# Performance work log

Measured on AMD Instinct MI355X. Metric: run time of the kernel, lower is better.

Reference implementation:

```python
import jax, jax.numpy as jnp
import numpy as np

ATTN_K = 64
H = 256  # seq_hidden_size


def setup_inputs() -> dict:
    key = jax.random.key(0)
    ks = jax.random.split(key, 10)
    N, Q = 1000000, 256
    return {
        "question": jax.random.normal(ks[0], (Q,), jnp.float32),
        "score": jax.random.uniform(ks[1], (), jnp.float32),
        "questions": jax.random.normal(ks[2], (N, Q), jnp.float32),
        "hs": jax.random.normal(ks[3], (N, H), jnp.float32),
        "W_score": jax.random.normal(ks[4], (1, Q + H), jnp.float32) * 0.05,
        "b_score": jax.random.normal(ks[5], (1,), jnp.float32) * 0.05,
        "W_ih": jax.random.normal(ks[6], (3 * H, 2 * Q), jnp.float32) * 0.05,
        "W_hh": jax.random.normal(ks[7], (3 * H, H), jnp.float32) * 0.05,
        "b_ih": jax.random.normal(ks[8], (3 * H,), jnp.float32) * 0.05,
        "b_hh": jax.random.normal(ks[9], (3 * H,), jnp.float32) * 0.05,
    }


def reference(question, score, questions, hs, W_score, b_score, W_ih, W_hh, b_ih, b_hh):
    # Attention over history: dot-product scores, top-k, softmax-weighted sum.
    alpha = questions @ question                      # [N]
    vals, idx = jax.lax.top_k(alpha, ATTN_K)          # [k], [k]
    w = jax.nn.softmax(vals)                          # softmax over the k selected scores
    attn_h = w @ hs[idx]                              # [H] weighted gather-sum

    # Score head on [question ; attn_h]
    pred_v = jnp.concatenate([question, attn_h])      # [Q+H]
    pred = W_score @ pred_v + b_score                 # [1]

    # GRU input: question gated by correctness of score
    right = (score >= 0.5).astype(question.dtype)
    x = jnp.concatenate([question * right, question * (1.0 - right)])  # [2Q]

    # Single GRU step (PyTorch gate ordering: r, z, n)
    h = hs[-1]                                        # [H]
    gx = W_ih @ x + b_ih                              # [3H]
    gh = W_hh @ h + b_hh                              # [3H]
    xr, xz, xn = gx[:H], gx[H:2 * H], gx[2 * H:]
    hr, hz, hn = gh[:H], gh[H:2 * H], gh[2 * H:]
    r = jax.nn.sigmoid(xr + hr)
    z = jax.nn.sigmoid(xz + hz)
    n = jnp.tanh(xn + r * hn)
    h_new = (1.0 - z) * n + z * h                     # [H]
    return pred, h_new
```

## Files before the change

### kernel.cpp

```cpp
#include <hip/hip_runtime.h>
#include <math.h>

#define Q 256
#define H 256
#define ATTN_K 64
#define CAP 4096
#define HBINS 4096

__device__ __forceinline__ unsigned f2k(float f) {
    unsigned u = __float_as_uint(f);
    return u ^ ((u & 0x80000000u) ? 0xFFFFFFFFu : 0x80000000u);
}

__global__ void k_setup(const float* __restrict__ question, const float* __restrict__ score,
                        const float* __restrict__ hs, const float* __restrict__ W_ih,
                        const float* __restrict__ W_hh, const float* __restrict__ b_ih,
                        const float* __restrict__ b_hh, float* __restrict__ gx,
                        float* __restrict__ gh, unsigned* __restrict__ hist,
                        unsigned* __restrict__ state, int N) {
    const int t = threadIdx.x;
    if (blockIdx.x < 16) hist[blockIdx.x * 256 + t] = 0u;
    if (blockIdx.x == 255 && t < 16) state[t] = 0u;

    const int o = blockIdx.x * 4 + (t >> 6);
    if (o >= 3 * H) return;
    const int lane = t & 63;
    const int off = (score[0] >= 0.5f) ? 0 : Q;
    const float4 q = *reinterpret_cast<const float4*>(question + lane * 4);
    const float4 h = *reinterpret_cast<const float4*>(hs + (size_t)(N - 1) * H + lane * 4);
    const float4 wx = *reinterpret_cast<const float4*>(W_ih + (size_t)o * (2 * Q) + off + lane * 4);
    const float4 wh = *reinterpret_cast<const float4*>(W_hh + (size_t)o * H + lane * 4);
    float px = wx.x * q.x + wx.y * q.y + wx.z * q.z + wx.w * q.w;
    float ph = wh.x * h.x + wh.y * h.y + wh.z * h.z + wh.w * h.w;
#pragma unroll
    for (int d = 32; d > 0; d >>= 1) {
        px += __shfl_xor(px, d, 64);
        ph += __shfl_xor(ph, d, 64);
    }
    if (lane == 0) {
        gx[o] = px + b_ih[o];
        gh[o] = ph + b_hh[o];
    }
}

__global__ __launch_bounds__(256) void k_alpha(const float* __restrict__ questions,
                                               const float* __restrict__ question,
                                               float* __restrict__ alpha, int N) {
    const int lane = threadIdx.x & 63;
    const int sub  = lane & 15;
    const int rg   = lane >> 4;
    const int wid  = (blockIdx.x * blockDim.x + threadIdx.x) >> 6;
    const int nw   = (gridDim.x * blockDim.x) >> 6;

    float4 q[4];
#pragma unroll
    for (int j = 0; j < 4; ++j)
        q[j] = *reinterpret_cast<const float4*>(question + j * 64 + sub * 4);

    for (int g = wid; g * 8 < N; g += nw) {
        const int rA = g * 8 + rg;
        const int rB = rA + 4;
        float pA = 0.f, pB = 0.f;
        if (rA < N) {
            const float* rowA = questions + (size_t)rA * Q + sub * 4;
#pragma unroll
            for (int j = 0; j < 4; ++j) {
                float4 x = *reinterpret_cast<const float4*>(rowA + j * 64);
                pA = fmaf(x.x, q[j].x, fmaf(x.y, q[j].y, fmaf(x.z, q[j].z, fmaf(x.w, q[j].w, pA))));
            }
        }
        if (rB < N) {
            const float* rowB = questions + (size_t)rB * Q + sub * 4;
#pragma unroll
            for (int j = 0; j < 4; ++j) {
                float4 x = *reinterpret_cast<const float4*>(rowB + j * 64);
                pB = fmaf(x.x, q[j].x, fmaf(x.y, q[j].y, fmaf(x.z, q[j].z, fmaf(x.w, q[j].w, pB))));
            }
        }
#pragma unroll
        for (int d = 1; d < 16; d <<= 1) {
            pA += __shfl_xor(pA, d, 64);
            pB += __shfl_xor(pB, d, 64);
        }
        if (sub == 0) {
            if (rA < N) alpha[rA] = pA;
            if (rB < N) alpha[rB] = pB;
        }
    }
}

__global__ __launch_bounds__(1024) void k_hist(const float* __restrict__ alpha,
                                               unsigned* __restrict__ hist, int N) {
    __shared__ unsigned hb[HBINS];
    const int t = threadIdx.x;
#pragma unroll
    for (int j = 0; j < HBINS / 1024; ++j) hb[t + j * 1024] = 0u;
    __syncthreads();

    const int n4 = N >> 2;
    const int stride = gridDim.x * blockDim.x;
    const float4* a4 = reinterpret_cast<const float4*>(alpha);
    for (int i = blockIdx.x * blockDim.x + t; i < n4; i += stride) {
        float4 a = a4[i];
        float v[4] = {a.x, a.y, a.z, a.w};
#pragma unroll
        for (int j = 0; j < 4; ++j) {
            int rel = (int)(f2k(v[j]) >> 19) - 4096;
            if (rel >= 0) atomicAdd(&hb[rel], 1u);
        }
    }
    if (blockIdx.x == 0 && t < (N & 3)) {
        float v = alpha[(n4 << 2) + t];
        int rel = (int)(f2k(v) >> 19) - 4096;
        if (rel >= 0) atomicAdd(&hb[rel], 1u);
    }
    __syncthreads();
#pragma unroll
    for (int j = 0; j < HBINS / 1024; ++j) {
        unsigned v = hb[t + j * 1024];
        if (v) atomicAdd(&hist[t + j * 1024], v);
    }
}

__global__ __launch_bounds__(1024) void k_scan(const unsigned* __restrict__ hist,
                                               unsigned* __restrict__ state) {
    __shared__ unsigned part[1024];
    __shared__ unsigned cum[1024];
    __shared__ int s_sh;
    const int t = threadIdx.x;

    {
        const int hi = 4095 - 4 * t;
        part[t] = hist[hi] + hist[hi - 1] + hist[hi - 2] + hist[hi - 3];
    }
    __syncthreads();
    cum[t] = part[t];
    __syncthreads();
    for (int d = 1; d < 1024; d <<= 1) {
        unsigned add = (t >= d) ? cum[t - d] : 0u;
        __syncthreads();
        if (t >= d) cum[t] += add;
        __syncthreads();
    }
    if (t == 0) s_sh = 1023;
    __syncthreads();
    if (cum[t] >= (unsigned)ATTN_K && (t == 0 || cum[t - 1] < (unsigned)ATTN_K)) s_sh = t;
    __syncthreads();
    if (t == 0) {
        const int s = s_sh;
        unsigned acc = (s > 0) ? cum[s - 1] : 0u;
        const int hi = 4095 - 4 * s;
        int tb = hi - 3;
        for (int b = hi; b >= hi - 3; --b) {
            acc += hist[b];
            if (acc >= (unsigned)ATTN_K) { tb = b; break; }
        }
        state[0] = (unsigned)(tb + 4096);
    }
}

__global__ void k_collect(const float* __restrict__ alpha, const unsigned* __restrict__ state,
                          float* __restrict__ cval, int* __restrict__ cidx,
                          unsigned* __restrict__ count, int N) {
    const int tau = (int)state[0];
    const int stride = gridDim.x * blockDim.x;
    const int n4 = N >> 2;
    const float4* a4 = reinterpret_cast<const float4*>(alpha);
    for (int i = blockIdx.x * blockDim.x + threadIdx.x; i < n4; i += stride) {
        float4 a = a4[i];
        float v[4] = {a.x, a.y, a.z, a.w};
#pragma unroll
        for (int j = 0; j < 4; ++j) {
            if ((int)(f2k(v[j]) >> 19) >= tau) {
                unsigned p = atomicAdd(count, 1u);
                if (p < CAP) { cval[p] = v[j]; cidx[p] = i * 4 + j; }
            }
        }
    }
    if (blockIdx.x == 0 && threadIdx.x < (N & 3)) {
        const int idx = (n4 << 2) + threadIdx.x;
        float v = alpha[idx];
        if ((int)(f2k(v) >> 19) >= tau) {
            unsigned p = atomicAdd(count, 1u);
            if (p < CAP) { cval[p] = v; cidx[p] = idx; }
        }
    }
}

__global__ void k_head(const float* __restrict__ question, const float* __restrict__ hs,
                       const float* __restrict__ W_score, const float* __restrict__ b_score,
                       const unsigned* __restrict__ state, const float* __restrict__ cval,
                       const int* __restrict__ cidx, const float* __restrict__ gx,
                       const float* __restrict__ gh, float* __restrict__ out, int N) {
    __shared__ float lv[CAP];
    __shared__ int li[CAP];
    __shared__ float sw[ATTN_K];
    __shared__ int si[ATTN_K];
    __shared__ float red[256];
    const int t = threadIdx.x;
    const int C = min((int)state[1], CAP);

    for (int i = t; i < C; i += 256) { lv[i] = cval[i]; li[i] = cidx[i]; }
    __syncthreads();

    if (t < 64) {
        for (int k = 0; k < ATTN_K; ++k) {
            float bv = -INFINITY;
            int bi = 0x7fffffff;
            int bp = -1;
            for (int i = t; i < C; i += 64) {
                float v = lv[i];
                int id = li[i];
                if (v > bv || (v == bv && id < bi)) { bv = v; bi = id; bp = i; }
            }
#pragma unroll
            for (int d = 32; d > 0; d >>= 1) {
                float ov = __shfl_xor(bv, d, 64);
                int oi = __shfl_xor(bi, d, 64);
                int op = __shfl_xor(bp, d, 64);
                if (ov > bv || (ov == bv && oi < bi)) { bv = ov; bi = oi; bp = op; }
            }
            if (t == 0) {
                sw[k] = bv;
                si[k] = (bi == 0x7fffffff) ? 0 : bi;
                if (bp >= 0) lv[bp] = -INFINITY;
            }
        }
        float m = sw[0];
        float e = expf(sw[t] - m);
        float ssum = e;
#pragma unroll
        for (int d = 32; d > 0; d >>= 1) ssum += __shfl_xor(ssum, d, 64);
        sw[t] = e / ssum;
    }
    __syncthreads();

    float aj = 0.f;
    for (int k = 0; k < ATTN_K; ++k) {
        aj = fmaf(sw[k], hs[(size_t)si[k] * H + t], aj);
    }

    red[t] = W_score[t] * question[t] + W_score[Q + t] * aj;
    __syncthreads();
    for (int d = 128; d > 0; d >>= 1) {
        if (t < d) red[t] += red[t + d];
        __syncthreads();
    }
    if (t == 0) out[0] = red[0] + b_score[0];

    {
        float xr = gx[t], xz = gx[H + t], xn = gx[2 * H + t];
        float hr = gh[t], hz = gh[H + t], hn = gh[2 * H + t];
        float r = 1.f / (1.f + expf(-(xr + hr)));
        float z = 1.f / (1.f + expf(-(xz + hz)));
        float n = tanhf(xn + r * hn);
        float hprev = hs[(size_t)(N - 1) * H + t];
        out[1 + t] = (1.f - z) * n + z * hprev;
    }
}

extern "C" void kernel_launch(void* const* d_in, const int* in_sizes, int n_in,
                              void* d_out, int out_size, void* d_ws, size_t ws_size,
                              hipStream_t stream) {
    const float* question = (const float*)d_in[0];
    const float* score    = (const float*)d_in[1];
    const float* questions= (const float*)d_in[2];
    const float* hs       = (const float*)d_in[3];
    const float* W_score  = (const float*)d_in[4];
    const float* b_score  = (const float*)d_in[5];
    const float* W_ih     = (const float*)d_in[6];
    const float* W_hh     = (const float*)d_in[7];
    const float* b_ih     = (const float*)d_in[8];
    const float* b_hh     = (const float*)d_in[9];
    const int N = in_sizes[2] / Q;
    float* out = (float*)d_out;

    char* ws = (char*)d_ws;
    size_t off = 0;
    float* alpha = (float*)(ws + off); off += (size_t)N * sizeof(float);
    off = (off + 255) & ~(size_t)255;
    unsigned* hist = (unsigned*)(ws + off); off += (size_t)HBINS * sizeof(unsigned);
    unsigned* state = (unsigned*)(ws + off); off += 256;
    float* cval = (float*)(ws + off); off += (size_t)CAP * sizeof(float);
    int* cidx = (int*)(ws + off); off += (size_t)CAP * sizeof(int);
    float* gx = (float*)(ws + off); off += 3 * H * sizeof(float);
    float* gh = (float*)(ws + off); off += 3 * H * sizeof(float);

    k_setup<<<256, 256, 0, stream>>>(question, score, hs, W_ih, W_hh, b_ih, b_hh,
                                     gx, gh, hist, state, N);
    k_alpha<<<2048, 256, 0, stream>>>(questions, question, alpha, N);
    k_hist<<<16, 1024, 0, stream>>>(alpha, hist, N);
    k_scan<<<1, 1024, 0, stream>>>(hist, state);
    k_collect<<<512, 256, 0, stream>>>(alpha, state, cval, cidx, state + 1, N);
    k_head<<<1, 256, 0, stream>>>(question, hs, W_score, b_score, state, cval, cidx,
                                  gx, gh, out, N);
}
```

Before: 268.5 us.

## Fuse six kernels into three with last-block-done patterns and nontemporal loads

Merges the GRU setup into the alpha dot-product kernel, folds the histogram scan into the histogram kernel, and folds the top-k head into the collect kernel. The last two fusions use an atomic counter so the final block to finish does the serial tail work. The questions stream now uses nontemporal loads with pointer-increment addressing, and the histogram grid grows from 16 to 64 blocks. This removes three launches and their gaps, and adds threadfence and atomic-counter synchronization in exchange.

Result: faster. 238.3 us (-11.2%).

```diff
diff --git a/kernel.cpp b/kernel.cpp
--- a/kernel.cpp
+++ b/kernel.cpp
@@ -7,73 +7,79 @@
 #define CAP 4096
 #define HBINS 4096
 
+typedef float f4 __attribute__((ext_vector_type(4)));
+
 __device__ __forceinline__ unsigned f2k(float f) {
     unsigned u = __float_as_uint(f);
     return u ^ ((u & 0x80000000u) ? 0xFFFFFFFFu : 0x80000000u);
 }
 
-__global__ void k_setup(const float* __restrict__ question, const float* __restrict__ score,
-                        const float* __restrict__ hs, const float* __restrict__ W_ih,
-                        const float* __restrict__ W_hh, const float* __restrict__ b_ih,
-                        const float* __restrict__ b_hh, float* __restrict__ gx,
-                        float* __restrict__ gh, unsigned* __restrict__ hist,
-                        unsigned* __restrict__ state, int N) {
+__global__ __launch_bounds__(256) void k_main(const float* __restrict__ questions,
+                                              const float* __restrict__ question,
+                                              const float* __restrict__ score,
+                                              const float* __restrict__ hs,
+                                              const float* __restrict__ W_ih,
+                                              const float* __restrict__ W_hh,
+                                              const float* __restrict__ b_ih,
+                                              const float* __restrict__ b_hh,
+                                              float* __restrict__ gx, float* __restrict__ gh,
+                                              unsigned* __restrict__ hist,
+                                              unsigned* __restrict__ state,
+                                              float* __restrict__ alpha, int N) {
     const int t = threadIdx.x;
-    if (blockIdx.x < 16) hist[blockIdx.x * 256 + t] = 0u;
-    if (blockIdx.x == 255 && t < 16) state[t] = 0u;
-
-    const int o = blockIdx.x * 4 + (t >> 6);
-    if (o >= 3 * H) return;
+    const int b = blockIdx.x;
+    if (b < 16) hist[b * 256 + t] = 0u;
+    if (b == 16 && t < 16) state[t] = 0u;
+
     const int lane = t & 63;
-    const int off = (score[0] >= 0.5f) ? 0 : Q;
-    const float4 q = *reinterpret_cast<const float4*>(question + lane * 4);
-    const float4 h = *reinterpret_cast<const float4*>(hs + (size_t)(N - 1) * H + lane * 4);
-    const float4 wx = *reinterpret_cast<const float4*>(W_ih + (size_t)o * (2 * Q) + off + lane * 4);
-    const float4 wh = *reinterpret_cast<const float4*>(W_hh + (size_t)o * H + lane * 4);
-    float px = wx.x * q.x + wx.y * q.y + wx.z * q.z + wx.w * q.w;
-    float ph = wh.x * h.x + wh.y * h.y + wh.z * h.z + wh.w * h.w;
-#pragma unroll
-    for (int d = 32; d > 0; d >>= 1) {
-        px += __shfl_xor(px, d, 64);
-        ph += __shfl_xor(ph, d, 64);
-    }
-    if (lane == 0) {
-        gx[o] = px + b_ih[o];
-        gh[o] = ph + b_hh[o];
-    }
-}
-
-__global__ __launch_bounds__(256) void k_alpha(const float* __restrict__ questions,
-                                               const float* __restrict__ question,
-                                               float* __restrict__ alpha, int N) {
-    const int lane = threadIdx.x & 63;
-    const int sub  = lane & 15;
-    const int rg   = lane >> 4;
-    const int wid  = (blockIdx.x * blockDim.x + threadIdx.x) >> 6;
-    const int nw   = (gridDim.x * blockDim.x) >> 6;
+    const int wid = b * 4 + (t >> 6);
+
+    if (wid < 3 * H) {
+        const int o = wid;
+        const int off = (score[0] >= 0.5f) ? 0 : Q;
+        const float4 q = *reinterpret_cast<const float4*>(question + lane * 4);
+        const float4 h = *reinterpret_cast<const float4*>(hs + (size_t)(N - 1) * H + lane * 4);
+        const float4 wx = *reinterpret_cast<const float4*>(W_ih + (size_t)o * (2 * Q) + off + lane * 4);
+        const float4 wh = *reinterpret_cast<const float4*>(W_hh + (size_t)o * H + lane * 4);
+        float px = wx.x * q.x + wx.y * q.y + wx.z * q.z + wx.w * q.w;
+        float ph = wh.x * h.x + wh.y * h.y + wh.z * h.z + wh.w * h.w;
+#pragma unroll
+        for (int d = 32; d > 0; d >>= 1) {
+            px += __shfl_xor(px, d, 64);
+            ph += __shfl_xor(ph, d, 64);
+        }
+        if (lane == 0) {
+            gx[o] = px + b_ih[o];
+            gh[o] = ph + b_hh[o];
+        }
+    }
+
+    const int sub = lane & 15;
+    const int rg  = lane >> 4;
+    const int nw  = (gridDim.x * blockDim.x) >> 6;
 
     float4 q[4];
 #pragma unroll
     for (int j = 0; j < 4; ++j)
         q[j] = *reinterpret_cast<const float4*>(question + j * 64 + sub * 4);
 
-    for (int g = wid; g * 8 < N; g += nw) {
-        const int rA = g * 8 + rg;
+    const size_t stepRows = (size_t)nw * 8;
+    const float* baseA = questions + (size_t)(wid * 8 + rg) * Q + sub * 4;
+    for (size_t r0 = (size_t)wid * 8; r0 < (size_t)N; r0 += stepRows, baseA += stepRows * Q) {
+        const int rA = (int)r0 + rg;
         const int rB = rA + 4;
         float pA = 0.f, pB = 0.f;
         if (rA < N) {
-            const float* rowA = questions + (size_t)rA * Q + sub * 4;
 #pragma unroll
             for (int j = 0; j < 4; ++j) {
-                float4 x = *reinterpret_cast<const float4*>(rowA + j * 64);
+                f4 x = __builtin_nontemporal_load(reinterpret_cast<const f4*>(baseA + j * 64));
                 pA = fmaf(x.x, q[j].x, fmaf(x.y, q[j].y, fmaf(x.z, q[j].z, fmaf(x.w, q[j].w, pA))));
             }
         }
         if (rB < N) {
-            const float* rowB = questions + (size_t)rB * Q + sub * 4;
 #pragma unroll
             for (int j = 0; j < 4; ++j) {
-                float4 x = *reinterpret_cast<const float4*>(rowB + j * 64);
+                f4 x = __builtin_nontemporal_load(reinterpret_cast<const f4*>(baseA + 4 * Q + j * 64));
                 pB = fmaf(x.x, q[j].x, fmaf(x.y, q[j].y, fmaf(x.z, q[j].z, fmaf(x.w, q[j].w, pB))));
             }
         }
@@ -89,9 +95,12 @@
     }
 }
 
-__global__ __launch_bounds__(1024) void k_hist(const float* __restrict__ alpha,
-                                               unsigned* __restrict__ hist, int N) {
+__global__ __launch_bounds__(1024) void k_histscan(const float* __restrict__ alpha,
+                                                   unsigned* __restrict__ hist,
+                                                   unsigned* __restrict__ state, int N) {
     __shared__ unsigned hb[HBINS];
+    __shared__ unsigned wsum[16];
+    __shared__ int flag_sh;
     const int t = threadIdx.x;
 #pragma unroll
     for (int j = 0; j < HBINS / 1024; ++j) hb[t + j * 1024] = 0u;
@@ -120,86 +129,109 @@
         unsigned v = hb[t + j * 1024];
         if (v) atomicAdd(&hist[t + j * 1024], v);
     }
-}
-
-__global__ __launch_bounds__(1024) void k_scan(const unsigned* __restrict__ hist,
-                                               unsigned* __restrict__ state) {
-    __shared__ unsigned part[1024];
-    __shared__ unsigned cum[1024];
-    __shared__ int s_sh;
-    const int t = threadIdx.x;
-
-    {
-        const int hi = 4095 - 4 * t;
-        part[t] = hist[hi] + hist[hi - 1] + hist[hi - 2] + hist[hi - 3];
-    }
-    __syncthreads();
-    cum[t] = part[t];
-    __syncthreads();
-    for (int d = 1; d < 1024; d <<= 1) {
-        unsigned add = (t >= d) ? cum[t - d] : 0u;
-        __syncthreads();
-        if (t >= d) cum[t] += add;
-        __syncthreads();
-    }
-    if (t == 0) s_sh = 1023;
-    __syncthreads();
-    if (cum[t] >= (unsigned)ATTN_K && (t == 0 || cum[t - 1] < (unsigned)ATTN_K)) s_sh = t;
-    __syncthreads();
+
     if (t == 0) {
-        const int s = s_sh;
-        unsigned acc = (s > 0) ? cum[s - 1] : 0u;
+        __threadfence();
+        unsigned a = atomicAdd(&state[3], 1u);
+        flag_sh = (a == gridDim.x - 1) ? 1 : 0;
+    }
+    __syncthreads();
+    if (!flag_sh) return;
+    __threadfence();
+
+    const uint4* h4 = reinterpret_cast<const uint4*>(hist);
+    uint4 hv = h4[1023 - t];
+    unsigned x = hv.x + hv.y + hv.z + hv.w;
+
+    const int lane = t & 63;
+    const int w = t >> 6;
+#pragma unroll
+    for (int d = 1; d < 64; d <<= 1) {
+        unsigned y = __shfl_up(x, d, 64);
+        if (lane >= d) x += y;
+    }
+    if (lane == 63) wsum[w] = x;
+    __syncthreads();
+    if (w == 0 && lane < 16) {
+        unsigned s = wsum[lane];
+#pragma unroll
+        for (int d = 1; d < 16; d <<= 1) {
+            unsigned y = __shfl_up(s, d, 64);
+            if (lane >= d) s += y;
+        }
+        wsum[lane] = s;
+    }
+    __syncthreads();
+    unsigned cum = x + ((w > 0) ? wsum[w - 1] : 0u);
+    hb[t] = cum;
+    __syncthreads();
+    if (cum >= (unsigned)ATTN_K && (t == 0 || hb[t - 1] < (unsigned)ATTN_K)) {
+        const int s = t;
+        unsigned acc = (s > 0) ? hb[s - 1] : 0u;
         const int hi = 4095 - 4 * s;
         int tb = hi - 3;
-        for (int b = hi; b >= hi - 3; --b) {
-            acc += hist[b];
-            if (acc >= (unsigned)ATTN_K) { tb = b; break; }
+        for (int bin = hi; bin >= hi - 3; --bin) {
+            acc += hist[bin];
+            if (acc >= (unsigned)ATTN_K) { tb = bin; break; }
         }
         state[0] = (unsigned)(tb + 4096);
     }
 }
 
-__global__ void k_collect(const float* __restrict__ alpha, const unsigned* __restrict__ state,
-                          float* __restrict__ cval, int* __restrict__ cidx,
-                          unsigned* __restrict__ count, int N) {
-    const int tau = (int)state[0];
-    const int stride = gridDim.x * blockDim.x;
-    const int n4 = N >> 2;
-    const float4* a4 = reinterpret_cast<const float4*>(alpha);
-    for (int i = blockIdx.x * blockDim.x + threadIdx.x; i < n4; i += stride) {
-        float4 a = a4[i];
-        float v[4] = {a.x, a.y, a.z, a.w};
-#pragma unroll
-        for (int j = 0; j < 4; ++j) {
-            if ((int)(f2k(v[j]) >> 19) >= tau) {
-                unsigned p = atomicAdd(count, 1u);
-                if (p < CAP) { cval[p] = v[j]; cidx[p] = i * 4 + j; }
-            }
-        }
-    }
-    if (blockIdx.x == 0 && threadIdx.x < (N & 3)) {
-        const int idx = (n4 << 2) + threadIdx.x;
-        float v = alpha[idx];
-        if ((int)(f2k(v) >> 19) >= tau) {
-            unsigned p = atomicAdd(count, 1u);
-            if (p < CAP) { cval[p] = v; cidx[p] = idx; }
-        }
-    }
-}
-
-__global__ void k_head(const float* __restrict__ question, const float* __restrict__ hs,
-                       const float* __restrict__ W_score, const float* __restrict__ b_score,
-                       const unsigned* __restrict__ state, const float* __restrict__ cval,
-                       const int* __restrict__ cidx, const float* __restrict__ gx,
-                       const float* __restrict__ gh, float* __restrict__ out, int N) {
+__global__ __launch_bounds__(256) void k_collecthead(const float* __restrict__ alpha,
+                                                     const float* __restrict__ question,
+                                                     const float* __restrict__ hs,
+                                                     const float* __restrict__ W_score,
+                                                     const float* __restrict__ b_score,
+                                                     unsigned* __restrict__ state,
+                                                     float* __restrict__ cval, int* __restrict__ cidx,
+                                                     const float* __restrict__ gx,
+                                                     const float* __restrict__ gh,
+                                                     float* __restrict__ out, int N) {
     __shared__ float lv[CAP];
     __shared__ int li[CAP];
     __shared__ float sw[ATTN_K];
     __shared__ int si[ATTN_K];
     __shared__ float red[256];
+    __shared__ int flag_sh;
     const int t = threadIdx.x;
+    const int tau = (int)state[0];
+
+    {
+        const int stride = gridDim.x * blockDim.x;
+        const int n4 = N >> 2;
+        const float4* a4 = reinterpret_cast<const float4*>(alpha);
+        for (int i = blockIdx.x * blockDim.x + t; i < n4; i += stride) {
+            float4 a = a4[i];
+            float v[4] = {a.x, a.y, a.z, a.w};
+#pragma unroll
+            for (int j = 0; j < 4; ++j) {
+                if ((int)(f2k(v[j]) >> 19) >= tau) {
+                    unsigned p = atomicAdd(&state[1], 1u);
+                    if (p < CAP) { cval[p] = v[j]; cidx[p] = i * 4 + j; }
+                }
+            }
+        }
+        if (blockIdx.x == 0 && t < (N & 3)) {
+            const int idx = (n4 << 2) + t;
+            float v = alpha[idx];
+            if ((int)(f2k(v) >> 19) >= tau) {
+                unsigned p = atomicAdd(&state[1], 1u);
+                if (p < CAP) { cval[p] = v; cidx[p] = idx; }
+            }
+        }
+    }
+
+    if (t == 0) {
+        __threadfence();
+        unsigned a = atomicAdd(&state[2], 1u);
+        flag_sh = (a == gridDim.x - 1) ? 1 : 0;
+    }
+    __syncthreads();
+    if (!flag_sh) return;
+    __threadfence();
+
     const int C = min((int)state[1], CAP);
-
     for (int i = t; i < C; i += 256) { lv[i] = cval[i]; li[i] = cidx[i]; }
     __syncthreads();
 
@@ -286,12 +318,9 @@
     float* gx = (float*)(ws + off); off += 3 * H * sizeof(float);
     float* gh = (float*)(ws + off); off += 3 * H * sizeof(float);
 
-    k_setup<<<256, 256, 0, stream>>>(question, score, hs, W_ih, W_hh, b_ih, b_hh,
-                                     gx, gh, hist, state, N);
-    k_alpha<<<2048, 256, 0, stream>>>(questions, question, alpha, N);
-    k_hist<<<16, 1024, 0, stream>>>(alpha, hist, N);
-    k_scan<<<1, 1024, 0, stream>>>(hist, state);
-    k_collect<<<512, 256, 0, stream>>>(alpha, state, cval, cidx, state + 1, N);
-    k_head<<<1, 256, 0, stream>>>(question, hs, W_score, b_score, state, cval, cidx,
-                                  gx, gh, out, N);
-}
+    k_main<<<2048, 256, 0, stream>>>(questions, question, score, hs, W_ih, W_hh,
+                                     b_ih, b_hh, gx, gh, hist, state, alpha, N);
+    k_histscan<<<64, 1024, 0, stream>>>(alpha, hist, state, N);
+    k_collecthead<<<512, 256, 0, stream>>>(alpha, question, hs, W_score, b_score,
+                                           state, cval, cidx, gx, gh, out, N);
+}
```
